# Kernel tuning notes

Hardware: AMD Instinct MI355X
Metric: run time of the kernel (lower is better)

The kernel has to match this reference:

```python
import jax, jax.numpy as jnp
import numpy as np

N = 50000      # nodes
E = 800000     # edges
F_IN = 128     # num_node_features
H = 128        # hidden_size
P = 128        # projection_dim
G = 512        # num graphs in batch


def setup_inputs() -> dict:
    key = jax.random.key(0)
    ks = jax.random.split(key, 16)
    def w(k, shape, fan_in):
        return (jax.random.normal(k, shape, jnp.float32) / np.float32(np.sqrt(fan_in)))
    inp = {
        "x": jax.random.normal(ks[0], (N, F_IN), jnp.float32),
        "edge_index": jax.random.randint(ks[1], (2, E), 0, N, dtype=jnp.int32),
        "batch": jnp.sort(jax.random.randint(ks[2], (N,), 0, G, dtype=jnp.int32)),
        "W_in": w(ks[3], (F_IN, H), F_IN), "b_in": jnp.zeros((H,), jnp.float32),
        "W1": w(ks[4], (H, H), H), "b1": jnp.zeros((H,), jnp.float32),
        "W2": w(ks[5], (H, H), H), "b2": jnp.zeros((H,), jnp.float32),
        "W3": w(ks[6], (H, H), H), "b3": jnp.zeros((H,), jnp.float32),
        "Wp1": w(ks[7], (3 * H, H), 3 * H), "bp1": jnp.zeros((H,), jnp.float32),
        "Wp2": w(ks[8], (H, P), H), "bp2": jnp.zeros((P,), jnp.float32),
    }
    return inp


def _gcn_conv(h_in, W, b, src, dst, dis):
    # GCNConv: D^-1/2 (A+I) D^-1/2 (X W) + b, edge weights = 1
    h = h_in @ W                                        # [N,H]
    norm = (dis[src] * dis[dst])[:, None]               # [E,1]
    msg = h[src] * norm                                 # gather + scale
    agg = jax.ops.segment_sum(msg, dst, num_segments=N)  # scatter-add
    agg = agg + h * (dis * dis)[:, None]                 # self-loop term
    return agg + b


def reference(x, edge_index, batch, W_in, b_in, W1, b1, W2, b2, W3, b3, Wp1, bp1, Wp2, bp2):
    src, dst = edge_index[0], edge_index[1]
    # degree with self-loops (target-side, symmetric norm)
    deg = jax.ops.segment_sum(jnp.ones((E,), jnp.float32), dst, num_segments=N) + 1.0
    dis = jax.lax.rsqrt(deg)                             # deg^-1/2, deg >= 1

    h = x @ W_in + b_in                                  # input projection
    r1 = jax.nn.relu(h + _gcn_conv(h, W1, b1, src, dst, dis))   # dropout = id (eval)
    r2 = jax.nn.relu(r1 + _gcn_conv(r1, W2, b2, src, dst, dis))
    r3 = jax.nn.relu(r2 + _gcn_conv(r2, W3, b3, src, dst, dis))

    jk = jnp.concatenate([r1, r2, r3], axis=1)           # JumpingKnowledge 'cat' -> [N,3H]
    sums = jax.ops.segment_sum(jk, batch, num_segments=G)
    cnts = jax.ops.segment_sum(jnp.ones((N,), jnp.float32), batch, num_segments=G)
    pooled = sums / jnp.maximum(cnts, 1.0)[:, None]      # global_mean_pool -> [G,3H]

    p = jax.nn.relu(pooled @ Wp1 + bp1) @ Wp2 + bp2      # projection head -> [G,P]
    nrm = jnp.sqrt(jnp.sum(p * p, axis=1, keepdims=True))
    return p / jnp.maximum(nrm, 1e-12)                   # F.normalize(dim=1)
```

## Files before the change

kernel.cpp:

```cpp
#include <hip/hip_runtime.h>
#include <hip/hip_bf16.h>


#define THREADS 256
#define BCAP 4096

typedef __attribute__((ext_vector_type(8))) short short8;
typedef __attribute__((ext_vector_type(4))) float f32x4;

static __device__ __forceinline__ unsigned short f2bf(float f) {
  unsigned u = __float_as_uint(f);
  u += 0x7fffu + ((u >> 16) & 1u);
  return (unsigned short)(u >> 16);
}
static __device__ __forceinline__ float bfval(unsigned short h) {
  return __uint_as_float((unsigned)h << 16);
}
static __device__ __forceinline__ float bf_lo(unsigned w) {
  return __uint_as_float(w << 16);
}
static __device__ __forceinline__ float bf_hi(unsigned w) {
  return __uint_as_float(w & 0xffff0000u);
}


__global__ __launch_bounds__(THREADS) void bucket_fill_kernel(
    const int* __restrict__ src, const int* __restrict__ dst,
    int* __restrict__ bkt_cursor, unsigned* __restrict__ edges_tmp, int E,
    const float* __restrict__ W0, const float* __restrict__ W1,
    const float* __restrict__ W2, const float* __restrict__ W3,
    unsigned short* __restrict__ Wtb) {
  __shared__ int hist[512];
  __shared__ int excl[512];
  __shared__ int gbase[512];
  __shared__ unsigned staging[2048];
  int t = threadIdx.x;
  int base = blockIdx.x * 2048;
  if (base >= E) {
    int cb = (E + 2047) >> 11;
    int tid = (blockIdx.x - cb) * THREADS + t;
    if (tid < 4 * 128 * 128) {
      int w = tid >> 14, c = (tid >> 7) & 127, k = tid & 127;
      const float* W = (w == 0) ? W0 : (w == 1) ? W1 : (w == 2) ? W2 : W3;
      float f = W[k * 128 + c];
      unsigned short hi = f2bf(f);
      unsigned short lo = f2bf(f - bfval(hi));
      int c16 = c >> 4, lc = c & 15;
      int ks = k >> 5, hq = (k >> 3) & 3, j = k & 7;
      int lane = hq * 16 + lc;
      size_t wb = (size_t)w * 32768;
      size_t fidx = (size_t)((c16 * 4 + ks) * 64 + lane) * 8 + j;
      Wtb[wb + fidx] = hi;
      Wtb[wb + 16384 + fidx] = lo;
    }
    return;
  }
  hist[t] = 0; hist[t + 256] = 0;
  __syncthreads();
  unsigned rec[8]; int bk[8]; int slot[8];
#pragma unroll
  for (int k = 0; k < 8; ++k) {
    int e = base + k * 256 + t;
    bk[k] = -1;
    if (e < E) {
      int d = dst[e];
      rec[k] = ((unsigned)d << 16) | (unsigned)src[e];
      bk[k] = d >> 7;
      slot[k] = atomicAdd(&hist[bk[k]], 1);
    }
  }
  __syncthreads();
  int v0 = hist[t], v1 = hist[t + 256];
  excl[t] = v0; excl[t + 256] = v1;
  __syncthreads();
  for (int off = 1; off < 512; off <<= 1) {
    int a = (t >= off) ? excl[t - off] : 0;
    int b = excl[t + 256 - off];
    __syncthreads();
    excl[t] += a; excl[t + 256] += b;
    __syncthreads();
  }
  int e0 = excl[t] - v0, e1 = excl[t + 256] - v1;
  __syncthreads();
  excl[t] = e0; excl[t + 256] = e1;
  __syncthreads();
#pragma unroll
  for (int k = 0; k < 8; ++k)
    if (bk[k] >= 0) staging[excl[bk[k]] + slot[k]] = rec[k];
  if (v0) gbase[t] = atomicAdd(&bkt_cursor[t], v0);
  if (v1) gbase[t + 256] = atomicAdd(&bkt_cursor[t + 256], v1);
  __syncthreads();
  int total = (base + 2048 <= E) ? 2048 : (E - base);
  for (int p = t; p < total; p += 256) {
    unsigned r = staging[p];
    int b = (int)(r >> 23);
    int pos = gbase[b] + (p - excl[b]);
    if (pos < BCAP)
      edges_tmp[(size_t)b * BCAP + pos] = r;
  }
}

__global__ __launch_bounds__(THREADS) void node_sort_kernel(
    const unsigned* __restrict__ edges_tmp, const int* __restrict__ bkt_cursor,
    const int* __restrict__ batch, int* __restrict__ row_beg,
    int* __restrict__ deg, float* __restrict__ dis,
    int* __restrict__ csr_src, int* __restrict__ g_off,
    unsigned* __restrict__ hwb_w, int N, int G) {
  __shared__ int lhist[128];
  __shared__ int lbase[128];
  __shared__ int lcur[128];
  int b = blockIdx.x, t = threadIdx.x;
  if (b == 0 && t >= 128 && t < 192)
    hwb_w[(size_t)N * 64 + (t - 128)] = 0;
  int cnt = bkt_cursor[b];
  if (cnt > BCAP) cnt = BCAP;
  size_t ebase = (size_t)b * BCAP;
  if (t < 128) lhist[t] = 0;
  __syncthreads();
  for (int p = t; p < cnt; p += 256)
    atomicAdd(&lhist[(edges_tmp[ebase + p] >> 16) & 127], 1);
  __syncthreads();
  int pad = 0;
  if (t < 128) {
    pad = (lhist[t] + 3) & ~3;
    lbase[t] = pad;
  }
  __syncthreads();
  for (int off = 1; off < 128; off <<= 1) {
    int a = (t >= off && t < 128) ? lbase[t - off] : 0;
    __syncthreads();
    if (t < 128) lbase[t] += a;
    __syncthreads();
  }
  if (t < 128) {
    int excl = lbase[t] - pad;
    int node = b * 128 + t;
    if (node < N) {
      row_beg[node] = (int)ebase + excl;
      deg[node] = lhist[t];
      dis[node] = rsqrtf((float)lhist[t] + 1.0f);
      for (int q = lhist[t]; q < pad; ++q)
        csr_src[ebase + excl + q] = N;
      int b0 = batch[node];
      int prev = (node == 0) ? -1 : batch[node - 1];
      for (int g = prev + 1; g <= b0; ++g) g_off[g] = node;
      if (node == N - 1)
        for (int g = b0 + 1; g <= G; ++g) g_off[g] = N;
    }
    lcur[t] = excl;
  }
  __syncthreads();
  for (int p = t; p < cnt; p += 256) {
    unsigned r = edges_tmp[ebase + p];
    int slot = atomicAdd(&lcur[(r >> 16) & 127], 1);
    csr_src[ebase + slot] = (int)(r & 0xffffu);
  }
}


template <int OUT_FP32>
__global__ __launch_bounds__(THREADS) void gemm_mfma(
    const float* __restrict__ A, const unsigned short* __restrict__ Wt,
    const float* __restrict__ bias, const float* __restrict__ scale,
    void* __restrict__ outv, int nrows) {
  __shared__ unsigned short lds[2][32][136];
  int t = threadIdx.x;
  int rbase = blockIdx.x * 32;
  if (rbase >= nrows) return;
#pragma unroll
  for (int i = 0; i < 4; ++i) {
    int fi = i * 256 + t;
    int row = fi >> 5;
    int c4 = fi & 31;
    int gr = rbase + row;
    f32x4 v = (gr < nrows) ? *(const f32x4*)&A[(size_t)gr * 128 + c4 * 4]
                           : (f32x4){0.f, 0.f, 0.f, 0.f};
    ushort4 hh, ll;
    unsigned short h0 = f2bf(v[0]); hh.x = h0; ll.x = f2bf(v[0] - bfval(h0));
    unsigned short h1 = f2bf(v[1]); hh.y = h1; ll.y = f2bf(v[1] - bfval(h1));
    unsigned short h2 = f2bf(v[2]); hh.z = h2; ll.z = f2bf(v[2] - bfval(h2));
    unsigned short h3 = f2bf(v[3]); hh.w = h3; ll.w = f2bf(v[3] - bfval(h3));
    *(ushort4*)&lds[0][row][c4 * 4] = hh;
    *(ushort4*)&lds[1][row][c4 * 4] = ll;
  }
  __syncthreads();
  int wave = t >> 6, lane = t & 63;
  int wr = wave >> 1, cw = wave & 1;
  int lrow = wr * 16 + (lane & 15);
  int hq = lane >> 4;
  int r = rbase + lrow;
  const short8* Wf = (const short8*)Wt;

  f32x4 acc[4];
#pragma unroll
  for (int i = 0; i < 4; ++i) acc[i] = (f32x4){0.f, 0.f, 0.f, 0.f};

#pragma unroll
  for (int ks = 0; ks < 4; ++ks) {
    short8 ahi = *(const short8*)&lds[0][lrow][ks * 32 + hq * 8];
    short8 alo = *(const short8*)&lds[1][lrow][ks * 32 + hq * 8];
#pragma unroll
    for (int i = 0; i < 4; ++i) {
      int c16 = cw * 4 + i;
      short8 wh = Wf[(c16 * 4 + ks) * 64 + lane];
      short8 wl = Wf[(32 + c16 * 4 + ks) * 64 + lane];
      acc[i] = __builtin_amdgcn_mfma_f32_16x16x32_bf16(wh, ahi, acc[i], 0, 0, 0);
      acc[i] = __builtin_amdgcn_mfma_f32_16x16x32_bf16(wl, ahi, acc[i], 0, 0, 0);
      acc[i] = __builtin_amdgcn_mfma_f32_16x16x32_bf16(wh, alo, acc[i], 0, 0, 0);
    }
  }

  if (r >= nrows) return;
  float sc = scale ? scale[r] : 1.0f;
#pragma unroll
  for (int i = 0; i < 4; ++i) {
    int fbase = cw * 64 + 16 * i + 4 * hq;
    float b4[4] = {0.f, 0.f, 0.f, 0.f};
    if (bias) {
      f32x4 bb = *(const f32x4*)&bias[fbase];
      b4[0] = bb[0]; b4[1] = bb[1]; b4[2] = bb[2]; b4[3] = bb[3];
    }
    if (OUT_FP32) {
      f32x4 o;
#pragma unroll
      for (int j = 0; j < 4; ++j) o[j] = (acc[i][j] + b4[j]) * sc;
      *(f32x4*)&((float*)outv)[(size_t)r * 128 + fbase] = o;
    } else {
      unsigned w0 = ((unsigned)f2bf((acc[i][1] + b4[1]) * sc) << 16) |
                    (unsigned)f2bf((acc[i][0] + b4[0]) * sc);
      unsigned w1 = ((unsigned)f2bf((acc[i][3] + b4[3]) * sc) << 16) |
                    (unsigned)f2bf((acc[i][2] + b4[2]) * sc);
      uint2 st; st.x = w0; st.y = w1;
      *(uint2*)&((unsigned short*)outv)[(size_t)r * 128 + fbase] = st;
    }
  }
}

__global__ __launch_bounds__(THREADS) void agg_kernel(
    const float* __restrict__ hin, const unsigned short* __restrict__ hwsb,
    const float* __restrict__ bias, const float* __restrict__ dis,
    const int* __restrict__ row_beg, const int* __restrict__ deg,
    const int* __restrict__ csr_src, float* __restrict__ out, int n) {
  int v = (blockIdx.x * THREADS + threadIdx.x) >> 6;
  int lane = threadIdx.x & 63;
  if (v >= n) return;
  int p = lane & 15;
  int qa = (lane >> 4) << 2;
  const char* hwB = (const char*)hwsb;
  float acc[8];
#pragma unroll
  for (int i = 0; i < 8; ++i) acc[i] = 0.f;
  int b = row_beg[v];
  int pc = (deg[v] + 3) & ~3;

  for (int chunk = 0; chunk < pc; chunk += 64) {
    int m = pc - chunk; if (m > 64) m = 64;
    int idx = csr_src[b + chunk + lane];
    for (int j = 0; j < m; j += 4) {
      int s = __builtin_amdgcn_ds_bpermute((j << 2) + qa, idx);
      uint4 w = *(const uint4*)(hwB + (size_t)s * 256 + p * 16);
      acc[0] += bf_lo(w.x); acc[1] += bf_hi(w.x);
      acc[2] += bf_lo(w.y); acc[3] += bf_hi(w.y);
      acc[4] += bf_lo(w.z); acc[5] += bf_hi(w.z);
      acc[6] += bf_lo(w.w); acc[7] += bf_hi(w.w);
    }
  }
#pragma unroll
  for (int i = 0; i < 8; ++i) {
    acc[i] += __shfl_xor(acc[i], 16, 64);
    acc[i] += __shfl_xor(acc[i], 32, 64);
  }
  if (lane < 16) {
    float dv = dis[v];
    uint4 sw = *(const uint4*)(hwB + (size_t)v * 256 + p * 16);
    float sf[8] = {bf_lo(sw.x), bf_hi(sw.x), bf_lo(sw.y), bf_hi(sw.y),
                   bf_lo(sw.z), bf_hi(sw.z), bf_lo(sw.w), bf_hi(sw.w)};
    f32x4 h0 = *(const f32x4*)&hin[(size_t)v * 128 + p * 8];
    f32x4 h1 = *(const f32x4*)&hin[(size_t)v * 128 + p * 8 + 4];
    f32x4 bb0 = *(const f32x4*)&bias[p * 8];
    f32x4 bb1 = *(const f32x4*)&bias[p * 8 + 4];
    f32x4 o0, o1;
#pragma unroll
    for (int j = 0; j < 4; ++j) {
      o0[j] = fmaxf(h0[j] + dv * (acc[j] + sf[j]) + bb0[j], 0.f);
      o1[j] = fmaxf(h1[j] + dv * (acc[4 + j] + sf[4 + j]) + bb1[j], 0.f);
    }
    *(f32x4*)&out[(size_t)v * 128 + p * 8] = o0;
    *(f32x4*)&out[(size_t)v * 128 + p * 8 + 4] = o1;
  }
}

__global__ __launch_bounds__(512) void pool_head_kernel(
    const float* __restrict__ r1, const float* __restrict__ r2,
    const float* __restrict__ r3, const int* __restrict__ g_off,
    const float* __restrict__ Wp1, const float* __restrict__ bp1,
    const float* __restrict__ Wp2, const float* __restrict__ bp2,
    float* __restrict__ out) {
  __shared__ float red[4][384];
  __shared__ float ps[384];
  __shared__ float t1[128];
  __shared__ float wsum[2];
  int g = blockIdx.x, t = threadIdx.x;
  int f = t & 127;
  int sub = t >> 7;
  int beg = g_off[g], end = g_off[g + 1];
  float s1 = 0.f, s2 = 0.f, s3 = 0.f;
  for (int i = beg + sub; i < end; i += 4) {
    size_t o = (size_t)i * 128 + f;
    s1 += r1[o]; s2 += r2[o]; s3 += r3[o];
  }
  red[sub][f] = s1; red[sub][128 + f] = s2; red[sub][256 + f] = s3;
  __syncthreads();
  float inv = 1.0f / fmaxf((float)(end - beg), 1.0f);
  if (t < 384)
    ps[t] = ((red[0][t] + red[1][t]) + (red[2][t] + red[3][t])) * inv;
  __syncthreads();
  if (t < 128) {
    float acc = bp1[t];
    for (int k = 0; k < 384; ++k) acc += ps[k] * Wp1[k * 128 + t];
    t1[t] = fmaxf(acc, 0.f);
  }
  __syncthreads();
  if (t < 128) {
    float acc2 = bp2[t];
    for (int k = 0; k < 128; ++k) acc2 += t1[k] * Wp2[k * 128 + t];
    float ss = acc2 * acc2;
    for (int off = 32; off > 0; off >>= 1) ss += __shfl_down(ss, off, 64);
    if ((t & 63) == 0) wsum[t >> 6] = ss;
    __syncthreads();
    float nrm = sqrtf(wsum[0] + wsum[1]);
    out[g * 128 + t] = acc2 / fmaxf(nrm, 1e-12f);
  }
}

static inline size_t align256(size_t x) { return (x + 255) & ~(size_t)255; }

extern "C" void kernel_launch(void* const* d_in, const int* in_sizes, int n_in,
                              void* d_out, int out_size, void* d_ws, size_t ws_size,
                              hipStream_t stream) {
  const float* x     = (const float*)d_in[0];
  const int*   ei    = (const int*)d_in[1];
  const int*   batch = (const int*)d_in[2];
  const float* W_in  = (const float*)d_in[3];
  const float* b_in  = (const float*)d_in[4];
  const float* W1    = (const float*)d_in[5];
  const float* b1    = (const float*)d_in[6];
  const float* W2    = (const float*)d_in[7];
  const float* b2    = (const float*)d_in[8];
  const float* W3    = (const float*)d_in[9];
  const float* b3    = (const float*)d_in[10];
  const float* Wp1   = (const float*)d_in[11];
  const float* bp1   = (const float*)d_in[12];
  const float* Wp2   = (const float*)d_in[13];
  const float* bp2   = (const float*)d_in[14];
  float* out = (float*)d_out;

  const int N = in_sizes[0] / 128;
  const int E = in_sizes[1] / 2;
  const int G = out_size / 128;
  const int* src = ei;
  const int* dst = ei + E;
  const int NB = (N + 127) / 128;
  const int CBLKS = (E + 2047) / 2048;

  char* p = (char*)d_ws;
  auto carve = [&](size_t bytes) { char* r = p; p += align256(bytes); return (void*)r; };
  int*   bkt_cursor = (int*)carve((size_t)NB * 4);
  int*   g_off      = (int*)carve((size_t)(G + 1) * 4);
  int*   row_beg    = (int*)carve((size_t)N * 4);
  int*   deg        = (int*)carve((size_t)N * 4);
  unsigned* edges_tmp = (unsigned*)carve((size_t)NB * BCAP * 4);
  int*   csr_src    = (int*)carve((size_t)NB * BCAP * 4);
  float* dis        = (float*)carve((size_t)N * 4);
  unsigned short* Wtb = (unsigned short*)carve((size_t)4 * 2 * 128 * 128 * 2);
  float* h   = (float*)carve((size_t)N * 128 * 4);
  float* r1  = (float*)carve((size_t)N * 128 * 4);
  float* r2  = (float*)carve((size_t)N * 128 * 4);
  float* r3  = (float*)carve((size_t)N * 128 * 4);
  unsigned short* hwb = (unsigned short*)carve((size_t)(N + 1) * 128 * 2);
  (void)ws_size; (void)n_in;

  hipMemsetAsync(bkt_cursor, 0, (size_t)NB * 4, stream);

  bucket_fill_kernel<<<CBLKS + 256, THREADS, 0, stream>>>(
      src, dst, bkt_cursor, edges_tmp, E, W_in, W1, W2, W3, Wtb);
  node_sort_kernel<<<NB, THREADS, 0, stream>>>(
      edges_tmp, bkt_cursor, batch, row_beg, deg, dis, csr_src, g_off,
      (unsigned*)hwb, N, G);

  int gemmBlocks = (N + 31) / 32;
  int aggBlocks = (N + 3) / 4;

  const unsigned short* Wt0 = Wtb;
  const unsigned short* Wt1 = Wtb + 32768;
  const unsigned short* Wt2 = Wtb + 2 * 32768;
  const unsigned short* Wt3 = Wtb + 3 * 32768;

  gemm_mfma<1><<<gemmBlocks, THREADS, 0, stream>>>(x, Wt0, b_in, nullptr, h, N);
  gemm_mfma<0><<<gemmBlocks, THREADS, 0, stream>>>(h, Wt1, nullptr, dis, hwb, N);
  agg_kernel<<<aggBlocks, THREADS, 0, stream>>>(h, hwb, b1, dis, row_beg, deg, csr_src, r1, N);
  gemm_mfma<0><<<gemmBlocks, THREADS, 0, stream>>>(r1, Wt2, nullptr, dis, hwb, N);
  agg_kernel<<<aggBlocks, THREADS, 0, stream>>>(r1, hwb, b2, dis, row_beg, deg, csr_src, r2, N);
  gemm_mfma<0><<<gemmBlocks, THREADS, 0, stream>>>(r2, Wt3, nullptr, dis, hwb, N);
  agg_kernel<<<aggBlocks, THREADS, 0, stream>>>(r2, hwb, b3, dis, row_beg, deg, csr_src, r3, N);

  pool_head_kernel<<<G, 512, 0, stream>>>(r1, r2, r3, g_off, Wp1, bp1, Wp2, bp2, out);
}
```

Measured before the change: 240.9 us.

## Fuse input projection with first conv GEMM; vectorize edge loads and pooling

Merges the input projection GEMM and the first GCN weight GEMM into one kernel. The intermediate h tile stays in LDS, split into bf16 hi/lo halves, so it is not re-read from global memory, and one launch goes away. The bucket-fill kernel now reads 8 contiguous edges per thread with int4 loads instead of strided scalar loads, which changes the order edges are staged in. The pooling kernel uses float4 loads and 16 row groups instead of 4. Together these cut memory traffic and launch overhead, at the cost of more LDS use and register pressure in the fused kernel.

```diff
diff --git a/kernel.cpp b/kernel.cpp
--- a/kernel.cpp
+++ b/kernel.cpp
@@ -57,15 +57,27 @@
   }
   hist[t] = 0; hist[t + 256] = 0;
   __syncthreads();
+  int e0 = base + t * 8;
+  int ds[8], ss[8];
+  if (e0 + 7 < E) {
+    *(int4*)&ds[0] = *(const int4*)&dst[e0];
+    *(int4*)&ds[4] = *(const int4*)&dst[e0 + 4];
+    *(int4*)&ss[0] = *(const int4*)&src[e0];
+    *(int4*)&ss[4] = *(const int4*)&src[e0 + 4];
+  } else {
+#pragma unroll
+    for (int k = 0; k < 8; ++k) {
+      ds[k] = (e0 + k < E) ? dst[e0 + k] : -1;
+      ss[k] = (e0 + k < E) ? src[e0 + k] : 0;
+    }
+  }
   unsigned rec[8]; int bk[8]; int slot[8];
 #pragma unroll
   for (int k = 0; k < 8; ++k) {
-    int e = base + k * 256 + t;
     bk[k] = -1;
-    if (e < E) {
-      int d = dst[e];
-      rec[k] = ((unsigned)d << 16) | (unsigned)src[e];
-      bk[k] = d >> 7;
+    if (ds[k] >= 0) {
+      rec[k] = ((unsigned)ds[k] << 16) | (unsigned)ss[k];
+      bk[k] = ds[k] >> 7;
       slot[k] = atomicAdd(&hist[bk[k]], 1);
     }
   }
@@ -80,9 +92,9 @@
     excl[t] += a; excl[t + 256] += b;
     __syncthreads();
   }
-  int e0 = excl[t] - v0, e1 = excl[t + 256] - v1;
-  __syncthreads();
-  excl[t] = e0; excl[t + 256] = e1;
+  int e0x = excl[t] - v0, e1x = excl[t + 256] - v1;
+  __syncthreads();
+  excl[t] = e0x; excl[t + 256] = e1x;
   __syncthreads();
 #pragma unroll
   for (int k = 0; k < 8; ++k)
@@ -158,11 +170,11 @@
 }
 
 
-template <int OUT_FP32>
-__global__ __launch_bounds__(THREADS) void gemm_mfma(
-    const float* __restrict__ A, const unsigned short* __restrict__ Wt,
-    const float* __restrict__ bias, const float* __restrict__ scale,
-    void* __restrict__ outv, int nrows) {
+__global__ __launch_bounds__(THREADS) void gemm_in_kernel(
+    const float* __restrict__ A, const unsigned short* __restrict__ Wt0,
+    const float* __restrict__ bias, const unsigned short* __restrict__ Wt1,
+    const float* __restrict__ dis, float* __restrict__ hout,
+    unsigned short* __restrict__ hwbout, int nrows) {
   __shared__ unsigned short lds[2][32][136];
   int t = threadIdx.x;
   int rbase = blockIdx.x * 32;
@@ -189,12 +201,111 @@
   int lrow = wr * 16 + (lane & 15);
   int hq = lane >> 4;
   int r = rbase + lrow;
+  const short8* Wf0 = (const short8*)Wt0;
+  const short8* Wf1 = (const short8*)Wt1;
+
+  f32x4 acc[4];
+#pragma unroll
+  for (int i = 0; i < 4; ++i) acc[i] = (f32x4){0.f, 0.f, 0.f, 0.f};
+#pragma unroll
+  for (int ks = 0; ks < 4; ++ks) {
+    short8 ahi = *(const short8*)&lds[0][lrow][ks * 32 + hq * 8];
+    short8 alo = *(const short8*)&lds[1][lrow][ks * 32 + hq * 8];
+#pragma unroll
+    for (int i = 0; i < 4; ++i) {
+      int c16 = cw * 4 + i;
+      short8 wh = Wf0[(c16 * 4 + ks) * 64 + lane];
+      short8 wl = Wf0[(32 + c16 * 4 + ks) * 64 + lane];
+      acc[i] = __builtin_amdgcn_mfma_f32_16x16x32_bf16(wh, ahi, acc[i], 0, 0, 0);
+      acc[i] = __builtin_amdgcn_mfma_f32_16x16x32_bf16(wl, ahi, acc[i], 0, 0, 0);
+      acc[i] = __builtin_amdgcn_mfma_f32_16x16x32_bf16(wh, alo, acc[i], 0, 0, 0);
+    }
+  }
+  __syncthreads();
+#pragma unroll
+  for (int i = 0; i < 4; ++i) {
+    int fbase = cw * 64 + 16 * i + 4 * hq;
+    f32x4 bb = *(const f32x4*)&bias[fbase];
+    f32x4 hv;
+#pragma unroll
+    for (int j = 0; j < 4; ++j) hv[j] = acc[i][j] + bb[j];
+    if (r < nrows)
+      *(f32x4*)&hout[(size_t)r * 128 + fbase] = hv;
+    ushort4 hh, ll;
+    unsigned short q0 = f2bf(hv[0]); hh.x = q0; ll.x = f2bf(hv[0] - bfval(q0));
+    unsigned short q1 = f2bf(hv[1]); hh.y = q1; ll.y = f2bf(hv[1] - bfval(q1));
+    unsigned short q2 = f2bf(hv[2]); hh.z = q2; ll.z = f2bf(hv[2] - bfval(q2));
+    unsigned short q3 = f2bf(hv[3]); hh.w = q3; ll.w = f2bf(hv[3] - bfval(q3));
+    *(ushort4*)&lds[0][lrow][fbase] = hh;
+    *(ushort4*)&lds[1][lrow][fbase] = ll;
+  }
+  __syncthreads();
+#pragma unroll
+  for (int i = 0; i < 4; ++i) acc[i] = (f32x4){0.f, 0.f, 0.f, 0.f};
+#pragma unroll
+  for (int ks = 0; ks < 4; ++ks) {
+    short8 ahi = *(const short8*)&lds[0][lrow][ks * 32 + hq * 8];
+    short8 alo = *(const short8*)&lds[1][lrow][ks * 32 + hq * 8];
+#pragma unroll
+    for (int i = 0; i < 4; ++i) {
+      int c16 = cw * 4 + i;
+      short8 wh = Wf1[(c16 * 4 + ks) * 64 + lane];
+      short8 wl = Wf1[(32 + c16 * 4 + ks) * 64 + lane];
+      acc[i] = __builtin_amdgcn_mfma_f32_16x16x32_bf16(wh, ahi, acc[i], 0, 0, 0);
+      acc[i] = __builtin_amdgcn_mfma_f32_16x16x32_bf16(wl, ahi, acc[i], 0, 0, 0);
+      acc[i] = __builtin_amdgcn_mfma_f32_16x16x32_bf16(wh, alo, acc[i], 0, 0, 0);
+    }
+  }
+  if (r >= nrows) return;
+  float sc = dis[r];
+#pragma unroll
+  for (int i = 0; i < 4; ++i) {
+    int fbase = cw * 64 + 16 * i + 4 * hq;
+    unsigned w0 = ((unsigned)f2bf(acc[i][1] * sc) << 16) |
+                  (unsigned)f2bf(acc[i][0] * sc);
+    unsigned w1 = ((unsigned)f2bf(acc[i][3] * sc) << 16) |
+                  (unsigned)f2bf(acc[i][2] * sc);
+    uint2 st; st.x = w0; st.y = w1;
+    *(uint2*)&hwbout[(size_t)r * 128 + fbase] = st;
+  }
+}
+
+template <int OUT_FP32>
+__global__ __launch_bounds__(THREADS) void gemm_mfma(
+    const float* __restrict__ A, const unsigned short* __restrict__ Wt,
+    const float* __restrict__ bias, const float* __restrict__ scale,
+    void* __restrict__ outv, int nrows) {
+  __shared__ unsigned short lds[2][32][136];
+  int t = threadIdx.x;
+  int rbase = blockIdx.x * 32;
+  if (rbase >= nrows) return;
+#pragma unroll
+  for (int i = 0; i < 4; ++i) {
+    int fi = i * 256 + t;
+    int row = fi >> 5;
+    int c4 = fi & 31;
+    int gr = rbase + row;
+    f32x4 v = (gr < nrows) ? *(const f32x4*)&A[(size_t)gr * 128 + c4 * 4]
+                           : (f32x4){0.f, 0.f, 0.f, 0.f};
+    ushort4 hh, ll;
+    unsigned short h0 = f2bf(v[0]); hh.x = h0; ll.x = f2bf(v[0] - bfval(h0));
+    unsigned short h1 = f2bf(v[1]); hh.y = h1; ll.y = f2bf(v[1] - bfval(h1));
+    unsigned short h2 = f2bf(v[2]); hh.z = h2; ll.z = f2bf(v[2] - bfval(h2));
+    unsigned short h3 = f2bf(v[3]); hh.w = h3; ll.w = f2bf(v[3] - bfval(h3));
+    *(ushort4*)&lds[0][row][c4 * 4] = hh;
+    *(ushort4*)&lds[1][row][c4 * 4] = ll;
+  }
+  __syncthreads();
+  int wave = t >> 6, lane = t & 63;
+  int wr = wave >> 1, cw = wave & 1;
+  int lrow = wr * 16 + (lane & 15);
+  int hq = lane >> 4;
+  int r = rbase + lrow;
   const short8* Wf = (const short8*)Wt;
 
   f32x4 acc[4];
 #pragma unroll
   for (int i = 0; i < 4; ++i) acc[i] = (f32x4){0.f, 0.f, 0.f, 0.f};
-
 #pragma unroll
   for (int ks = 0; ks < 4; ++ks) {
     short8 ahi = *(const short8*)&lds[0][lrow][ks * 32 + hq * 8];
@@ -209,7 +320,6 @@
       acc[i] = __builtin_amdgcn_mfma_f32_16x16x32_bf16(wh, alo, acc[i], 0, 0, 0);
     }
   }
-
   if (r >= nrows) return;
   float sc = scale ? scale[r] : 1.0f;
 #pragma unroll
@@ -296,24 +406,37 @@
     const float* __restrict__ Wp1, const float* __restrict__ bp1,
     const float* __restrict__ Wp2, const float* __restrict__ bp2,
     float* __restrict__ out) {
-  __shared__ float red[4][384];
+  __shared__ float red[16][384];
   __shared__ float ps[384];
   __shared__ float t1[128];
   __shared__ float wsum[2];
   int g = blockIdx.x, t = threadIdx.x;
-  int f = t & 127;
-  int sub = t >> 7;
+  int sub = t >> 5;
+  int c4 = t & 31;
   int beg = g_off[g], end = g_off[g + 1];
-  float s1 = 0.f, s2 = 0.f, s3 = 0.f;
-  for (int i = beg + sub; i < end; i += 4) {
-    size_t o = (size_t)i * 128 + f;
-    s1 += r1[o]; s2 += r2[o]; s3 += r3[o];
-  }
-  red[sub][f] = s1; red[sub][128 + f] = s2; red[sub][256 + f] = s3;
-  __syncthreads();
-  float inv = 1.0f / fmaxf((float)(end - beg), 1.0f);
-  if (t < 384)
-    ps[t] = ((red[0][t] + red[1][t]) + (red[2][t] + red[3][t])) * inv;
+  f32x4 s1 = {0.f, 0.f, 0.f, 0.f}, s2 = s1, s3 = s1;
+  for (int i = beg + sub; i < end; i += 16) {
+    size_t o = (size_t)i * 128 + c4 * 4;
+    f32x4 a = *(const f32x4*)&r1[o];
+    f32x4 b = *(const f32x4*)&r2[o];
+    f32x4 c = *(const f32x4*)&r3[o];
+#pragma unroll
+    for (int j = 0; j < 4; ++j) { s1[j] += a[j]; s2[j] += b[j]; s3[j] += c[j]; }
+  }
+#pragma unroll
+  for (int j = 0; j < 4; ++j) {
+    red[sub][c4 * 4 + j] = s1[j];
+    red[sub][128 + c4 * 4 + j] = s2[j];
+    red[sub][256 + c4 * 4 + j] = s3[j];
+  }
+  __syncthreads();
+  if (t < 384) {
+    float inv = 1.0f / fmaxf((float)(end - beg), 1.0f);
+    float s = 0.f;
+#pragma unroll
+    for (int k = 0; k < 16; ++k) s += red[k][t];
+    ps[t] = s * inv;
+  }
   __syncthreads();
   if (t < 128) {
     float acc = bp1[t];
@@ -396,8 +519,8 @@
   const unsigned short* Wt2 = Wtb + 2 * 32768;
   const unsigned short* Wt3 = Wtb + 3 * 32768;
 
-  gemm_mfma<1><<<gemmBlocks, THREADS, 0, stream>>>(x, Wt0, b_in, nullptr, h, N);
-  gemm_mfma<0><<<gemmBlocks, THREADS, 0, stream>>>(h, Wt1, nullptr, dis, hwb, N);
+  gemm_in_kernel<<<gemmBlocks, THREADS, 0, stream>>>(
+      x, Wt0, b_in, Wt1, dis, h, hwb, N);
   agg_kernel<<<aggBlocks, THREADS, 0, stream>>>(h, hwb, b1, dis, row_beg, deg, csr_src, r1, N);
   gemm_mfma<0><<<gemmBlocks, THREADS, 0, stream>>>(r1, Wt2, nullptr, dis, hwb, N);
   agg_kernel<<<aggBlocks, THREADS, 0, stream>>>(r1, hwb, b2, dis, row_beg, deg, csr_src, r2, N);
```

Result: faster. 232.9 us (-3.3%).
